# Kernel optimization log

Measured on AMD Instinct MI355X. Metric: run time of the kernel, lower is better.

## Reference

```python
import jax, jax.numpy as jnp
import numpy as np

B, S, D = 2, 2048, 768
H = 12
HD = D // H


def setup_inputs() -> dict:
    key = jax.random.key(0)
    ks = jax.random.split(key, 9)
    s_in = 1.0 / np.sqrt(D)
    return {
        "x": jax.random.normal(ks[0], (B, S, D), dtype=jnp.float32),
        "wq": jax.random.normal(ks[1], (D, D), dtype=jnp.float32) * s_in,
        "bq": jax.random.normal(ks[2], (D,), dtype=jnp.float32) * 0.01,
        "wk": jax.random.normal(ks[3], (D, D), dtype=jnp.float32) * s_in,
        "bk": jax.random.normal(ks[4], (D,), dtype=jnp.float32) * 0.01,
        "wv": jax.random.normal(ks[5], (D, D), dtype=jnp.float32) * s_in,
        "bv": jax.random.normal(ks[6], (D,), dtype=jnp.float32) * 0.01,
        "wo": jax.random.normal(ks[7], (D, D), dtype=jnp.float32) * s_in,
        "bo": jax.random.normal(ks[8], (D,), dtype=jnp.float32) * 0.01,
    }


def reference(x, wq, bq, wk, bk, wv, bv, wo, bo):
    b, s, _ = x.shape
    # projections -> [b, h, s, hd]
    def proj(w, bias):
        return (x @ w + bias).reshape(b, s, H, HD).transpose(0, 2, 1, 3)
    q = proj(wq, bq)
    k = proj(wk, bk)
    v = proj(wv, bv)
    scores = jnp.einsum("bhqd,bhkd->bhqk", q, k)
    causal = jnp.triu(jnp.ones((s, s), dtype=bool), k=1)
    scores = jnp.where(causal, -jnp.inf, scores)
    attn = jax.nn.softmax(scores / np.sqrt(HD), axis=-1)
    # dropout p=0.0 -> identity
    ctx = jnp.einsum("bhqk,bhkd->bhqd", attn, v)
    ctx = ctx.transpose(0, 2, 1, 3).reshape(b, s, D)
    return ctx @ wo + bo
```

## Files before the change

### kernel.cpp

```cpp
#include <hip/hip_runtime.h>
#include <math.h>

#define BB  2
#define SS  2048
#define DD  768
#define HH  12
#define HDD 64
#define BSR (BB * SS)
#define NCH 40
#define NKT 12

typedef __attribute__((ext_vector_type(8))) short bf16x8;
typedef __attribute__((ext_vector_type(4))) float f32x4;
typedef __attribute__((ext_vector_type(4))) int  i32x4;

__device__ inline f32x4 mfma16(bf16x8 a, bf16x8 b, f32x4 c) {
    return __builtin_amdgcn_mfma_f32_16x16x32_bf16(a, b, c, 0, 0, 0);
}

__device__ inline unsigned short f2b(float f) {
    unsigned int u = __float_as_uint(f);
    u += 0x7FFFu + ((u >> 16) & 1u);
    return (unsigned short)(u >> 16);
}
__device__ inline float b2f(unsigned short u) {
    return __uint_as_float((unsigned int)u << 16);
}

__device__ inline unsigned int cvt_pk_bf16(float lo, float hi) {
    unsigned int r;
    asm("v_cvt_pk_bf16_f32 %0, %1, %2" : "=v"(r) : "v"(lo), "v"(hi));
    return r;
}

__device__ inline void async_copy16(void* lds, const void* g) {
    __builtin_amdgcn_global_load_lds(
        (const __attribute__((address_space(1))) unsigned int*)g,
        (__attribute__((address_space(3))) unsigned int*)lds, 16, 0, 0);
}

__global__ __launch_bounds__(256) void conv_x_kernel(
    const float* __restrict__ x, unsigned short* __restrict__ xb)
{
    const size_t i = ((size_t)blockIdx.x * 256 + threadIdx.x) * 8;
    float4 f0 = *(const float4*)&x[i];
    float4 f1 = *(const float4*)&x[i + 4];
    i32x4 tv;
    tv[0] = (int)cvt_pk_bf16(f0.x, f0.y);
    tv[1] = (int)cvt_pk_bf16(f0.z, f0.w);
    tv[2] = (int)cvt_pk_bf16(f1.x, f1.y);
    tv[3] = (int)cvt_pk_bf16(f1.z, f1.w);
    *(i32x4*)&xb[i] = tv;
}

__global__ __launch_bounds__(256) void conv_wT_kernel(
    const float* __restrict__ w0, const float* __restrict__ w1,
    const float* __restrict__ w2, const float* __restrict__ w3,
    unsigned short* __restrict__ o0, unsigned short* __restrict__ o1,
    unsigned short* __restrict__ o2, unsigned short* __restrict__ o3)
{
    const float* w = (blockIdx.z == 0) ? w0 : (blockIdx.z == 1) ? w1
                   : (blockIdx.z == 2) ? w2 : w3;
    unsigned short* o = (blockIdx.z == 0) ? o0 : (blockIdx.z == 1) ? o1
                      : (blockIdx.z == 2) ? o2 : o3;
    const int n0 = blockIdx.x * 64;
    const int k0 = blockIdx.y * 64;
    const int tid = threadIdx.x;

    __shared__ unsigned short tile[64][72];

#pragma unroll
    for (int p = 0; p < 4; ++p) {
        int c  = p * 256 + tid;
        int kr = c >> 4;
        int nc = (c & 15) * 4;
        float4 v = *(const float4*)&w[(size_t)(k0 + kr) * DD + n0 + nc];
        tile[nc + 0][kr] = f2b(v.x);
        tile[nc + 1][kr] = f2b(v.y);
        tile[nc + 2][kr] = f2b(v.z);
        tile[nc + 3][kr] = f2b(v.w);
    }
    __syncthreads();
#pragma unroll
    for (int p = 0; p < 2; ++p) {
        int c  = p * 256 + tid;
        int nr = c >> 3;
        int kc = (c & 7) * 8;
        *(i32x4*)&o[(size_t)(n0 + nr) * DD + k0 + kc] = *(const i32x4*)&tile[nr][kc];
    }
}

__global__ __launch_bounds__(256) void qkv_gemm_kernel(
    const unsigned short* __restrict__ xb,
    const unsigned short* __restrict__ wqT, const unsigned short* __restrict__ wkT,
    const unsigned short* __restrict__ wvT,
    const float* __restrict__ bq, const float* __restrict__ bk,
    const float* __restrict__ bv,
    unsigned short* __restrict__ Qg, unsigned short* __restrict__ Kg,
    unsigned short* __restrict__ Vg)
{
    const int p0   = blockIdx.x;
    const int xcd  = p0 & 7;
    const int slot = p0 >> 3;
    const int m_t  = (slot / 18) * 8 + xcd;
    const int nw   = slot % 18;
    const int n_t  = nw / 3;
    const int which = nw % 3;

    const unsigned short* Bt = (which == 0) ? wqT : (which == 1) ? wkT : wvT;
    const float* bias        = (which == 0) ? bq  : (which == 1) ? bk  : bv;
    unsigned short* out      = (which == 0) ? Qg  : (which == 1) ? Kg  : Vg;
    const float qs           = (which == 0) ? 0.18033688011112042f : 1.0f;

    const int m0 = m_t * 64;
    const int n0 = n_t * 128;
    const int tid  = threadIdx.x;
    const int w    = tid >> 6;
    const int lane = tid & 63;
    const int quad = lane >> 4;
    const int l16  = lane & 15;
    const int mh   = w & 1;
    const int nh   = w >> 1;
    const int swz  = l16 & 7;

    __shared__ unsigned short smem[24576];
    unsigned short (*As0)[64] = (unsigned short(*)[64])smem;
    unsigned short (*Bs0)[64] = (unsigned short(*)[64])(smem + 4096);
    unsigned short (*As1)[64] = (unsigned short(*)[64])(smem + 12288);
    unsigned short (*Bs1)[64] = (unsigned short(*)[64])(smem + 16384);
    unsigned short (*T)[136]  = (unsigned short(*)[136])smem;

    const unsigned short* gA[2];
    int ldsA[2];
#pragma unroll
    for (int p = 0; p < 2; ++p) {
        int c  = p * 256 + tid;
        int r  = c >> 3;
        int j  = c & 7;
        int ch = j ^ (r & 7);
        gA[p]   = &xb[(size_t)(m0 + r) * DD + ch * 8];
        ldsA[p] = r * 64 + j * 8;
    }
    const unsigned short* gB[4];
    int ldsB[4];
#pragma unroll
    for (int p = 0; p < 4; ++p) {
        int c  = p * 256 + tid;
        int r  = c >> 3;
        int j  = c & 7;
        int ch = j ^ (r & 7);
        gB[p]   = &Bt[(size_t)(n0 + r) * DD + ch * 8];
        ldsB[p] = r * 64 + j * 8;
    }

    f32x4 zero = {0.f, 0.f, 0.f, 0.f};
    f32x4 acc[2][4];
#pragma unroll
    for (int i = 0; i < 2; ++i)
#pragma unroll
        for (int j = 0; j < 4; ++j) acc[i][j] = zero;

#pragma unroll
    for (int p = 0; p < 2; ++p) async_copy16((unsigned short*)As0 + ldsA[p], gA[p]);
#pragma unroll
    for (int p = 0; p < 4; ++p) async_copy16((unsigned short*)Bs0 + ldsB[p], gB[p]);
    __syncthreads();

#pragma unroll
    for (int t = 0; t < NKT; ++t) {
        const int kn = (t + 1) * 64;
        unsigned short (*As)[64] = (t & 1) ? As1 : As0;
        unsigned short (*Bs)[64] = (t & 1) ? Bs1 : Bs0;
        unsigned short (*An)[64] = (t & 1) ? As0 : As1;
        unsigned short (*Bn)[64] = (t & 1) ? Bs0 : Bs1;
        if (t + 1 < NKT) {
#pragma unroll
            for (int p = 0; p < 2; ++p)
                async_copy16((unsigned short*)An + ldsA[p], gA[p] + kn);
#pragma unroll
            for (int p = 0; p < 4; ++p)
                async_copy16((unsigned short*)Bn + ldsB[p], gB[p] + kn);
        }
        bf16x8 af0[2], af1[2], bf0[4], bf1[4];
#pragma unroll
        for (int mt = 0; mt < 2; ++mt) {
            int r = mh * 32 + mt * 16 + l16;
            af0[mt] = *(const bf16x8*)&As[r][((quad    ) ^ swz) * 8];
            af1[mt] = *(const bf16x8*)&As[r][((quad + 4) ^ swz) * 8];
        }
#pragma unroll
        for (int nt = 0; nt < 4; ++nt) {
            int r = nh * 64 + nt * 16 + l16;
            bf0[nt] = *(const bf16x8*)&Bs[r][((quad    ) ^ swz) * 8];
            bf1[nt] = *(const bf16x8*)&Bs[r][((quad + 4) ^ swz) * 8];
        }
#pragma unroll
        for (int mt = 0; mt < 2; ++mt)
#pragma unroll
            for (int nt = 0; nt < 4; ++nt) {
                acc[mt][nt] = mfma16(af0[mt], bf0[nt], acc[mt][nt]);
                acc[mt][nt] = mfma16(af1[mt], bf1[nt], acc[mt][nt]);
            }
        __syncthreads();
    }

    if (which < 2) {
#pragma unroll
        for (int nt = 0; nt < 4; ++nt) {
            const int col = nh * 64 + nt * 16 + l16;
            const float bvv = bias[n0 + col];
#pragma unroll
            for (int mt = 0; mt < 2; ++mt)
#pragma unroll
                for (int r = 0; r < 4; ++r)
                    T[mh * 32 + mt * 16 + quad * 4 + r][col] =
                        f2b((acc[mt][nt][r] + bvv) * qs);
        }
        __syncthreads();
#pragma unroll
        for (int p2 = 0; p2 < 4; ++p2) {
            int c    = p2 * 256 + tid;
            int row  = c >> 4;
            int ck   = c & 15;
            int head = ck >> 3;
            int wi   = ck & 7;
            int sg   = m0 + row;
            int bi   = sg >> 11, si = sg & 2047;
            int hcol = (n0 >> 6) + head;
            *(i32x4*)&out[(((size_t)(bi * HH + hcol)) * SS + si) * HDD + wi * 8] =
                *(const i32x4*)&T[row][head * 64 + wi * 8];
        }
    } else {
        for (int pass = 0; pass < 2; ++pass) {
            if (pass) __syncthreads();
            if (nh == pass) {
#pragma unroll
                for (int nt = 0; nt < 4; ++nt) {
                    const float bvv = bias[n0 + pass * 64 + nt * 16 + l16];
#pragma unroll
                    for (int mt = 0; mt < 2; ++mt) {
                        uint2 pk;
                        pk.x = cvt_pk_bf16(acc[mt][nt][0] + bvv, acc[mt][nt][1] + bvv);
                        pk.y = cvt_pk_bf16(acc[mt][nt][2] + bvv, acc[mt][nt][3] + bvv);
                        *(uint2*)&T[nt * 16 + l16][mh * 32 + mt * 16 + quad * 4] = pk;
                    }
                }
            }
            __syncthreads();
            const int bi   = m0 >> 11;
            const int s0   = m0 & 2047;
            const int hcol = (n0 >> 6) + pass;
#pragma unroll
            for (int p2 = 0; p2 < 2; ++p2) {
                int c    = p2 * 256 + tid;
                int drow = c >> 3;
                int wi   = c & 7;
                *(i32x4*)&out[(((size_t)(bi * HH + hcol)) * HDD + drow) * SS + s0 + wi * 8] =
                    *(const i32x4*)&T[drow][wi * 8];
            }
        }
    }
}

__global__ __launch_bounds__(256) void out_gemm_kernel(
    const unsigned short* __restrict__ cb, const unsigned short* __restrict__ woT,
    const float* __restrict__ bo, float* __restrict__ out)
{
    const int p0   = blockIdx.x;
    const int xcd  = p0 & 7;
    const int slot = p0 >> 3;
    const int m0 = ((slot / 6) * 8 + xcd) * 64;
    const int n0 = (slot % 6) * 128;
    const int tid  = threadIdx.x;
    const int w    = tid >> 6;
    const int lane = tid & 63;
    const int quad = lane >> 4;
    const int l16  = lane & 15;
    const int mh   = w & 1;
    const int nh   = w >> 1;
    const int swz  = l16 & 7;

    __shared__ unsigned short smem[24576];
    unsigned short (*As0)[64] = (unsigned short(*)[64])smem;
    unsigned short (*Bs0)[64] = (unsigned short(*)[64])(smem + 4096);
    unsigned short (*As1)[64] = (unsigned short(*)[64])(smem + 12288);
    unsigned short (*Bs1)[64] = (unsigned short(*)[64])(smem + 16384);

    const unsigned short* gA[2];
    int ldsA[2];
#pragma unroll
    for (int p = 0; p < 2; ++p) {
        int c  = p * 256 + tid;
        int r  = c >> 3;
        int j  = c & 7;
        int ch = j ^ (r & 7);
        gA[p]   = &cb[(size_t)(m0 + r) * DD + ch * 8];
        ldsA[p] = r * 64 + j * 8;
    }
    const unsigned short* gB[4];
    int ldsB[4];
#pragma unroll
    for (int p = 0; p < 4; ++p) {
        int c  = p * 256 + tid;
        int r  = c >> 3;
        int j  = c & 7;
        int ch = j ^ (r & 7);
        gB[p]   = &woT[(size_t)(n0 + r) * DD + ch * 8];
        ldsB[p] = r * 64 + j * 8;
    }

    f32x4 zero = {0.f, 0.f, 0.f, 0.f};
    f32x4 acc[2][4];
#pragma unroll
    for (int i = 0; i < 2; ++i)
#pragma unroll
        for (int j = 0; j < 4; ++j) acc[i][j] = zero;

#pragma unroll
    for (int p = 0; p < 2; ++p) async_copy16((unsigned short*)As0 + ldsA[p], gA[p]);
#pragma unroll
    for (int p = 0; p < 4; ++p) async_copy16((unsigned short*)Bs0 + ldsB[p], gB[p]);
    __syncthreads();

#pragma unroll
    for (int t = 0; t < NKT; ++t) {
        const int kn = (t + 1) * 64;
        unsigned short (*As)[64] = (t & 1) ? As1 : As0;
        unsigned short (*Bs)[64] = (t & 1) ? Bs1 : Bs0;
        unsigned short (*An)[64] = (t & 1) ? As0 : As1;
        unsigned short (*Bn)[64] = (t & 1) ? Bs0 : Bs1;
        if (t + 1 < NKT) {
#pragma unroll
            for (int p = 0; p < 2; ++p)
                async_copy16((unsigned short*)An + ldsA[p], gA[p] + kn);
#pragma unroll
            for (int p = 0; p < 4; ++p)
                async_copy16((unsigned short*)Bn + ldsB[p], gB[p] + kn);
        }
        bf16x8 af0[2], af1[2], bf0[4], bf1[4];
#pragma unroll
        for (int mt = 0; mt < 2; ++mt) {
            int r = mh * 32 + mt * 16 + l16;
            af0[mt] = *(const bf16x8*)&As[r][((quad    ) ^ swz) * 8];
            af1[mt] = *(const bf16x8*)&As[r][((quad + 4) ^ swz) * 8];
        }
#pragma unroll
        for (int nt = 0; nt < 4; ++nt) {
            int r = nh * 64 + nt * 16 + l16;
            bf0[nt] = *(const bf16x8*)&Bs[r][((quad    ) ^ swz) * 8];
            bf1[nt] = *(const bf16x8*)&Bs[r][((quad + 4) ^ swz) * 8];
        }
#pragma unroll
        for (int mt = 0; mt < 2; ++mt)
#pragma unroll
            for (int nt = 0; nt < 4; ++nt) {
                acc[mt][nt] = mfma16(af0[mt], bf0[nt], acc[mt][nt]);
                acc[mt][nt] = mfma16(af1[mt], bf1[nt], acc[mt][nt]);
            }
        __syncthreads();
    }

#pragma unroll
    for (int nt = 0; nt < 4; ++nt) {
        const int n = n0 + nh * 64 + nt * 16 + l16;
        const float bvv = bo[n];
#pragma unroll
        for (int mt = 0; mt < 2; ++mt) {
            const int mbase = m0 + mh * 32 + mt * 16 + quad * 4;
#pragma unroll
            for (int r = 0; r < 4; ++r)
                out[(size_t)(mbase + r) * DD + n] = acc[mt][nt][r] + bvv;
        }
    }
}

__global__ __launch_bounds__(256, 4) void attn_mfma_kernel(
    const unsigned short* __restrict__ Qg, const unsigned short* __restrict__ Kg,
    const unsigned short* __restrict__ Vg, unsigned short* __restrict__ Opart,
    float* __restrict__ Lb)
{
    const int p0   = blockIdx.x;
    const int xcd  = p0 & 7;
    const int slot = p0 >> 3;
    const int bh_i = (slot / 40) * 8 + xcd;
    const int b    = bh_i / HH;
    const int h    = bh_i % HH;
    const int c    = (NCH - 1) - (slot % 40);

    int qt, ck, nch;
    if (c < 4)       { qt = c;                            ck = 0;     nch = 1; }
    else if (c < 12) { int t = c - 4;  qt = 4  + (t >> 1); ck = t & 1; nch = 2; }
    else if (c < 24) { int t = c - 12; qt = 8  + t / 3;    ck = t % 3; nch = 3; }
    else             { int t = c - 24; qt = 12 + (t >> 2); ck = t & 3; nch = 4; }
    const int NT   = 2 * qt + 2;
    const int base = NT / nch, rem = NT % nch;
    const int lo   = ck * base + min(ck, rem);
    const int hi   = lo + base + (ck < rem ? 1 : 0);
    const int dlo  = 2 * qt;

    const int tid  = threadIdx.x;
    const int w    = tid >> 6;
    const int lane = tid & 63;
    const int quad = lane >> 4;
    const int l16  = lane & 15;
    const int q0   = qt * 128;

    const size_t bh = (size_t)bh_i;
    const unsigned short* qp = Qg + bh * SS * HDD;
    const unsigned short* kp = Kg + bh * SS * HDD;
    const unsigned short* vp = Vg + bh * HDD * SS;

    unsigned short* op = Opart + ((size_t)bh * NCH + c) * 128 * HDD;
    float* lp = Lb + ((size_t)bh * NCH + c) * 128;

    __shared__ unsigned short Ks[64][64];
    __shared__ unsigned short Vt[64][64];
    __shared__ unsigned short PsT[4][2][16][72];
    unsigned short* slab = &PsT[w][0][0][0];

    bf16x8 qb0[2], qb1[2];
    int query[2];
#pragma unroll
    for (int qf = 0; qf < 2; ++qf) {
        query[qf] = q0 + w * 32 + qf * 16 + l16;
        qb0[qf] = *(const bf16x8*)&qp[(size_t)query[qf] * HDD + quad * 8];
        qb1[qf] = *(const bf16x8*)&qp[(size_t)query[qf] * HDD + 32 + quad * 8];
    }

    const int pr  = tid >> 3;
    const int po8 = tid & 7;
    const int fs  = l16 & 7;

    i32x4 kpre[2], vpre[2];
#pragma unroll
    for (int p = 0; p < 2; ++p) {
        int r  = pr + p * 32;
        int gc = (po8 ^ (r & 7)) * 8;
        kpre[p] = *(const i32x4*)&kp[(size_t)(lo * 64 + r) * HDD + gc];
        vpre[p] = *(const i32x4*)&vp[(size_t)r * SS + lo * 64 + gc];
    }

    f32x4 zero = {0.f, 0.f, 0.f, 0.f};
    f32x4 o_acc[2][4];
    float l_i[2] = {0.f, 0.f};
#pragma unroll
    for (int qf = 0; qf < 2; ++qf)
#pragma unroll
        for (int i = 0; i < 4; ++i) o_acc[qf][i] = zero;

    for (int kt = lo; kt < hi; ++kt) {
        const int k0 = kt * 64;
        __syncthreads();
#pragma unroll
        for (int p = 0; p < 2; ++p) {
            int r = pr + p * 32;
            *(i32x4*)&Ks[r][po8 * 8] = kpre[p];
            *(i32x4*)&Vt[r][po8 * 8] = vpre[p];
        }
        __syncthreads();

        if (kt + 1 < hi) {
            const int kn = (kt + 1) * 64;
#pragma unroll
            for (int p = 0; p < 2; ++p) {
                int r  = pr + p * 32;
                int gc = (po8 ^ (r & 7)) * 8;
                kpre[p] = *(const i32x4*)&kp[(size_t)(kn + r) * HDD + gc];
                vpre[p] = *(const i32x4*)&vp[(size_t)r * SS + kn + gc];
            }
        }

        const bool diag = (kt >= dlo);
#pragma unroll
        for (int t = 0; t < 4; ++t) {
            const int row = t * 16 + l16;
            bf16x8 klo = *(const bf16x8*)&Ks[row][((quad    ) ^ fs) * 8];
            bf16x8 khi = *(const bf16x8*)&Ks[row][((quad + 4) ^ fs) * 8];
#pragma unroll
            for (int qf = 0; qf < 2; ++qf) {
                f32x4 s = mfma16(klo, qb0[qf], zero);
                s = mfma16(khi, qb1[qf], s);
                float pv[4];
#pragma unroll
                for (int r = 0; r < 4; ++r) {
                    const int key = k0 + t * 16 + quad * 4 + r;
                    float p = exp2f(s[r]);
                    if (diag && key > query[qf]) p = 0.f;
                    pv[r] = p;
                    l_i[qf] += p;
                }
                uint2 pk;
                pk.x = cvt_pk_bf16(pv[0], pv[1]);
                pk.y = cvt_pk_bf16(pv[2], pv[3]);
                *(uint2*)&slab[(qf * 16 + l16) * 72 + t * 16 + quad * 4] = pk;
            }
        }

        bf16x8 pb0[2], pb1[2];
#pragma unroll
        for (int qf = 0; qf < 2; ++qf) {
            pb0[qf] = *(const bf16x8*)&slab[(qf * 16 + l16) * 72 + quad * 8];
            pb1[qf] = *(const bf16x8*)&slab[(qf * 16 + l16) * 72 + 32 + quad * 8];
        }
#pragma unroll
        for (int t2 = 0; t2 < 4; ++t2) {
            const int row = t2 * 16 + l16;
            bf16x8 vlo = *(const bf16x8*)&Vt[row][((quad    ) ^ fs) * 8];
            bf16x8 vhi = *(const bf16x8*)&Vt[row][((quad + 4) ^ fs) * 8];
#pragma unroll
            for (int qf = 0; qf < 2; ++qf) {
                o_acc[qf][t2] = mfma16(vlo, pb0[qf], o_acc[qf][t2]);
                o_acc[qf][t2] = mfma16(vhi, pb1[qf], o_acc[qf][t2]);
            }
        }
    }

#pragma unroll
    for (int qf = 0; qf < 2; ++qf) {
        float l = l_i[qf];
        l += __shfl_xor(l, 16);
        l += __shfl_xor(l, 32);
        if (quad == 0) lp[w * 32 + qf * 16 + l16] = l;
#pragma unroll
        for (int t2 = 0; t2 < 4; ++t2) {
            uint2 pk;
            pk.x = cvt_pk_bf16(o_acc[qf][t2][0], o_acc[qf][t2][1]);
            pk.y = cvt_pk_bf16(o_acc[qf][t2][2], o_acc[qf][t2][3]);
            *(uint2*)&slab[(qf * 16 + l16) * 72 + t2 * 16 + quad * 4] = pk;
        }
    }
#pragma unroll
    for (int p2 = 0; p2 < 4; ++p2) {
        int cc  = p2 * 64 + lane;
        int row = cc >> 3, dc = cc & 7;
        *(i32x4*)&op[(size_t)(w * 32 + row) * HDD + dc * 8] =
            *(const i32x4*)&slab[row * 72 + dc * 8];
    }
}

__global__ __launch_bounds__(256) void merge_kernel(
    const unsigned short* __restrict__ Opart, const float* __restrict__ Lb,
    unsigned short* __restrict__ cb)
{
    const int bx   = blockIdx.x;
    const int qt2  = bx >> 1;
    const int half = bx & 1;
    const int bhn  = blockIdx.y;
    const int b    = bhn / HH, h = bhn % HH;
    const int tid  = threadIdx.x;
    const int row  = tid >> 2;
    const int d0   = (tid & 3) * 16;
    const int rowc = half * 64 + row;
    const int q    = qt2 * 128 + rowc;

    const int nch = (qt2 < 4) ? 1 : (qt2 < 8) ? 2 : (qt2 < 12) ? 3 : 4;
    const int cb0 = (qt2 < 4) ? qt2
                  : (qt2 < 8)  ? (4  + (qt2 - 4)  * 2)
                  : (qt2 < 12) ? (12 + (qt2 - 8)  * 3)
                  :              (24 + (qt2 - 12) * 4);

    float suml = 0.f;
    float accv[16];
#pragma unroll
    for (int i = 0; i < 16; ++i) accv[i] = 0.f;

    for (int ci = 0; ci < nch; ++ci) {
        const size_t base = (size_t)bhn * NCH + cb0 + ci;
        suml += Lb[base * 128 + rowc];
        const unsigned short* o = Opart + (base * 128 + rowc) * HDD + d0;
        i32x4 va = *(const i32x4*)&o[0];
        i32x4 vb = *(const i32x4*)&o[8];
#pragma unroll
        for (int wd = 0; wd < 4; ++wd) {
            unsigned int ua = (unsigned int)va[wd];
            accv[wd * 2 + 0] += __uint_as_float(ua << 16);
            accv[wd * 2 + 1] += __uint_as_float(ua & 0xffff0000u);
            unsigned int ub = (unsigned int)vb[wd];
            accv[8 + wd * 2 + 0] += __uint_as_float(ub << 16);
            accv[8 + wd * 2 + 1] += __uint_as_float(ub & 0xffff0000u);
        }
    }
    const float inv = 1.0f / suml;
    unsigned int res[8];
#pragma unroll
    for (int i = 0; i < 8; ++i)
        res[i] = cvt_pk_bf16(accv[2 * i] * inv, accv[2 * i + 1] * inv);
    unsigned short* dst = &cb[((size_t)(b * SS + q)) * DD + h * HDD + d0];
    *(i32x4*)&dst[0] = *(const i32x4*)&res[0];
    *(i32x4*)&dst[8] = *(const i32x4*)&res[4];
}

extern "C" void kernel_launch(void* const* d_in, const int* in_sizes, int n_in,
                              void* d_out, int out_size, void* d_ws, size_t ws_size,
                              hipStream_t stream)
{
    const float* x  = (const float*)d_in[0];
    const float* wq = (const float*)d_in[1];
    const float* bq = (const float*)d_in[2];
    const float* wk = (const float*)d_in[3];
    const float* bk = (const float*)d_in[4];
    const float* wv = (const float*)d_in[5];
    const float* bv = (const float*)d_in[6];
    const float* wo = (const float*)d_in[7];
    const float* bo = (const float*)d_in[8];
    float* out = (float*)d_out;

    char* p = (char*)d_ws;
    const size_t XB  = (size_t)BSR * DD * 2;
    const size_t WB  = (size_t)DD * DD * 2;
    const size_t OPB = (size_t)BB * HH * NCH * 128 * HDD * 2;
    const size_t LBB = (size_t)BB * HH * NCH * 128 * 4;
    unsigned short* wqT = (unsigned short*)p;            p += WB;
    unsigned short* wkT = (unsigned short*)p;            p += WB;
    unsigned short* wvT = (unsigned short*)p;            p += WB;
    unsigned short* woT = (unsigned short*)p;            p += WB;
    unsigned short* xb  = (unsigned short*)p;            p += XB;
    unsigned short* Qg  = (unsigned short*)p;            p += XB;
    unsigned short* Kg  = (unsigned short*)p;            p += XB;
    unsigned short* Vg  = (unsigned short*)p;            p += XB;
    unsigned short* cb  = (unsigned short*)p;            p += XB;
    unsigned short* Opart = (unsigned short*)p;          p += OPB;
    float* Lb = (float*)p;                               p += LBB;

    conv_x_kernel<<<dim3(BSR * DD / (256 * 8)), 256, 0, stream>>>(x, xb);
    conv_wT_kernel<<<dim3(DD / 64, DD / 64, 4), 256, 0, stream>>>(
        wq, wk, wv, wo, wqT, wkT, wvT, woT);
    qkv_gemm_kernel<<<dim3(1152), 256, 0, stream>>>(
        xb, wqT, wkT, wvT, bq, bk, bv, Qg, Kg, Vg);
    attn_mfma_kernel<<<dim3(960), 256, 0, stream>>>(
        Qg, Kg, Vg, Opart, Lb);
    merge_kernel<<<dim3(32, BB * HH), 256, 0, stream>>>(Opart, Lb, cb);
    out_gemm_kernel<<<dim3(384), 256, 0, stream>>>(cb, woT, bo, out);
}
```

Measured before the change: 153.2 us.

## Double-buffer K/V shared tiles in attention and split diagonal mask path

Turns the single K/V shared-memory tile into a two-slot ping-pong buffer. The next tile is written to shared memory and the tile after that is prefetched into registers while the current tile is being computed, which cuts the two block barriers per key tile down to one. The causal mask check now runs only on diagonal tiles, and launch bounds drop from 4 to 3 blocks per SM. The larger LDS footprint and lower occupancy target may reduce how many blocks stay resident at once.

```diff
diff --git a/kernel.cpp b/kernel.cpp
--- a/kernel.cpp
+++ b/kernel.cpp
@@ -374,7 +374,7 @@
     }
 }
 
-__global__ __launch_bounds__(256, 4) void attn_mfma_kernel(
+__global__ __launch_bounds__(256, 3) void attn_mfma_kernel(
     const unsigned short* __restrict__ Qg, const unsigned short* __restrict__ Kg,
     const unsigned short* __restrict__ Vg, unsigned short* __restrict__ Opart,
     float* __restrict__ Lb)
@@ -383,8 +383,6 @@
     const int xcd  = p0 & 7;
     const int slot = p0 >> 3;
     const int bh_i = (slot / 40) * 8 + xcd;
-    const int b    = bh_i / HH;
-    const int h    = bh_i % HH;
     const int c    = (NCH - 1) - (slot % 40);
 
     int qt, ck, nch;
@@ -413,8 +411,8 @@
     unsigned short* op = Opart + ((size_t)bh * NCH + c) * 128 * HDD;
     float* lp = Lb + ((size_t)bh * NCH + c) * 128;
 
-    __shared__ unsigned short Ks[64][64];
-    __shared__ unsigned short Vt[64][64];
+    __shared__ unsigned short Ks[2][64][64];
+    __shared__ unsigned short Vt[2][64][64];
     __shared__ unsigned short PsT[4][2][16][72];
     unsigned short* slab = &PsT[w][0][0][0];
 
@@ -439,6 +437,23 @@
         kpre[p] = *(const i32x4*)&kp[(size_t)(lo * 64 + r) * HDD + gc];
         vpre[p] = *(const i32x4*)&vp[(size_t)r * SS + lo * 64 + gc];
     }
+#pragma unroll
+    for (int p = 0; p < 2; ++p) {
+        int r = pr + p * 32;
+        *(i32x4*)&Ks[0][r][po8 * 8] = kpre[p];
+        *(i32x4*)&Vt[0][r][po8 * 8] = vpre[p];
+    }
+    if (lo + 1 < hi) {
+        const int kn = (lo + 1) * 64;
+#pragma unroll
+        for (int p = 0; p < 2; ++p) {
+            int r  = pr + p * 32;
+            int gc = (po8 ^ (r & 7)) * 8;
+            kpre[p] = *(const i32x4*)&kp[(size_t)(kn + r) * HDD + gc];
+            vpre[p] = *(const i32x4*)&vp[(size_t)r * SS + kn + gc];
+        }
+    }
+    __syncthreads();
 
     f32x4 zero = {0.f, 0.f, 0.f, 0.f};
     f32x4 o_acc[2][4];
@@ -449,24 +464,26 @@
         for (int i = 0; i < 4; ++i) o_acc[qf][i] = zero;
 
     for (int kt = lo; kt < hi; ++kt) {
-        const int k0 = kt * 64;
-        __syncthreads();
-#pragma unroll
-        for (int p = 0; p < 2; ++p) {
-            int r = pr + p * 32;
-            *(i32x4*)&Ks[r][po8 * 8] = kpre[p];
-            *(i32x4*)&Vt[r][po8 * 8] = vpre[p];
-        }
-        __syncthreads();
+        const int k0   = kt * 64;
+        const int bufc = (kt - lo) & 1;
+        const int bufn = bufc ^ 1;
 
         if (kt + 1 < hi) {
-            const int kn = (kt + 1) * 64;
 #pragma unroll
             for (int p = 0; p < 2; ++p) {
-                int r  = pr + p * 32;
-                int gc = (po8 ^ (r & 7)) * 8;
-                kpre[p] = *(const i32x4*)&kp[(size_t)(kn + r) * HDD + gc];
-                vpre[p] = *(const i32x4*)&vp[(size_t)r * SS + kn + gc];
+                int r = pr + p * 32;
+                *(i32x4*)&Ks[bufn][r][po8 * 8] = kpre[p];
+                *(i32x4*)&Vt[bufn][r][po8 * 8] = vpre[p];
+            }
+            if (kt + 2 < hi) {
+                const int kn = (kt + 2) * 64;
+#pragma unroll
+                for (int p = 0; p < 2; ++p) {
+                    int r  = pr + p * 32;
+                    int gc = (po8 ^ (r & 7)) * 8;
+                    kpre[p] = *(const i32x4*)&kp[(size_t)(kn + r) * HDD + gc];
+                    vpre[p] = *(const i32x4*)&vp[(size_t)r * SS + kn + gc];
+                }
             }
         }
 
@@ -474,20 +491,28 @@
 #pragma unroll
         for (int t = 0; t < 4; ++t) {
             const int row = t * 16 + l16;
-            bf16x8 klo = *(const bf16x8*)&Ks[row][((quad    ) ^ fs) * 8];
-            bf16x8 khi = *(const bf16x8*)&Ks[row][((quad + 4) ^ fs) * 8];
+            bf16x8 klo = *(const bf16x8*)&Ks[bufc][row][((quad    ) ^ fs) * 8];
+            bf16x8 khi = *(const bf16x8*)&Ks[bufc][row][((quad + 4) ^ fs) * 8];
 #pragma unroll
             for (int qf = 0; qf < 2; ++qf) {
                 f32x4 s = mfma16(klo, qb0[qf], zero);
                 s = mfma16(khi, qb1[qf], s);
                 float pv[4];
-#pragma unroll
-                for (int r = 0; r < 4; ++r) {
-                    const int key = k0 + t * 16 + quad * 4 + r;
-                    float p = exp2f(s[r]);
-                    if (diag && key > query[qf]) p = 0.f;
-                    pv[r] = p;
-                    l_i[qf] += p;
+                if (!diag) {
+#pragma unroll
+                    for (int r = 0; r < 4; ++r) {
+                        pv[r] = exp2f(s[r]);
+                        l_i[qf] += pv[r];
+                    }
+                } else {
+#pragma unroll
+                    for (int r = 0; r < 4; ++r) {
+                        const int key = k0 + t * 16 + quad * 4 + r;
+                        float p = exp2f(s[r]);
+                        if (key > query[qf]) p = 0.f;
+                        pv[r] = p;
+                        l_i[qf] += p;
+                    }
                 }
                 uint2 pk;
                 pk.x = cvt_pk_bf16(pv[0], pv[1]);
@@ -505,14 +530,16 @@
 #pragma unroll
         for (int t2 = 0; t2 < 4; ++t2) {
             const int row = t2 * 16 + l16;
-            bf16x8 vlo = *(const bf16x8*)&Vt[row][((quad    ) ^ fs) * 8];
-            bf16x8 vhi = *(const bf16x8*)&Vt[row][((quad + 4) ^ fs) * 8];
+            bf16x8 vlo = *(const bf16x8*)&Vt[bufc][row][((quad    ) ^ fs) * 8];
+            bf16x8 vhi = *(const bf16x8*)&Vt[bufc][row][((quad + 4) ^ fs) * 8];
 #pragma unroll
             for (int qf = 0; qf < 2; ++qf) {
                 o_acc[qf][t2] = mfma16(vlo, pb0[qf], o_acc[qf][t2]);
                 o_acc[qf][t2] = mfma16(vhi, pb1[qf], o_acc[qf][t2]);
             }
         }
+
+        if (kt + 1 < hi) __syncthreads();
     }
 
 #pragma unroll
```

Measured after the change: 156.4 us. 1.02x slower.

## Fuse split-KV merge into output projection GEMM A-tile loading

Applied to the files above, without the earlier changes.

Removes the separate merge kernel and the cb context buffer. The output GEMM now reads partial attention outputs and row sums directly, combines and normalises them in registers, and writes the bf16 A tile into shared memory, prefetching the next head's partials during the current MFMA step. This saves one launch and a global round trip for the context tensor. In exchange, the GEMM's A loads become synchronous register loads with extra ALU work, replacing async copies, and each row's merge is redone by all six N-column blocks.

```diff
diff --git a/kernel.cpp b/kernel.cpp
--- a/kernel.cpp
+++ b/kernel.cpp
@@ -263,7 +263,8 @@
 }
 
 __global__ __launch_bounds__(256) void out_gemm_kernel(
-    const unsigned short* __restrict__ cb, const unsigned short* __restrict__ woT,
+    const unsigned short* __restrict__ Opart, const float* __restrict__ Lb,
+    const unsigned short* __restrict__ woT,
     const float* __restrict__ bo, float* __restrict__ out)
 {
     const int p0   = blockIdx.x;
@@ -280,23 +281,33 @@
     const int nh   = w >> 1;
     const int swz  = l16 & 7;
 
+    const int bi   = m0 >> 11;
+    const int s0   = m0 & 2047;
+    const int qt2  = s0 >> 7;
+    const int half = (s0 >> 6) & 1;
+    const int nch = (qt2 < 4) ? 1 : (qt2 < 8) ? 2 : (qt2 < 12) ? 3 : 4;
+    const int cb0 = (qt2 < 4) ? qt2
+                  : (qt2 < 8)  ? (4  + (qt2 - 4)  * 2)
+                  : (qt2 < 12) ? (12 + (qt2 - 8)  * 3)
+                  :              (24 + (qt2 - 12) * 4);
+
     __shared__ unsigned short smem[24576];
     unsigned short (*As0)[64] = (unsigned short(*)[64])smem;
     unsigned short (*Bs0)[64] = (unsigned short(*)[64])(smem + 4096);
     unsigned short (*As1)[64] = (unsigned short(*)[64])(smem + 12288);
     unsigned short (*Bs1)[64] = (unsigned short(*)[64])(smem + 16384);
 
-    const unsigned short* gA[2];
-    int ldsA[2];
-#pragma unroll
-    for (int p = 0; p < 2; ++p) {
-        int c  = p * 256 + tid;
-        int r  = c >> 3;
-        int j  = c & 7;
-        int ch = j ^ (r & 7);
-        gA[p]   = &cb[(size_t)(m0 + r) * DD + ch * 8];
-        ldsA[p] = r * 64 + j * 8;
-    }
+    const int arow = tid >> 2;
+    const int ad0  = (tid & 3) * 16;
+    const int aj0  = ad0 >> 3;
+    const int aw0  = arow * 64 + ((aj0      ^ (arow & 7)) * 8);
+    const int aw1  = arow * 64 + (((aj0 + 1) ^ (arow & 7)) * 8);
+    const size_t rstep = (size_t)NCH * 128;
+    size_t rbase[4];
+#pragma unroll
+    for (int ci = 0; ci < 4; ++ci)
+        rbase[ci] = ((size_t)(bi * HH) * NCH + cb0 + ci) * 128 + half * 64 + arow;
+
     const unsigned short* gB[4];
     int ldsB[4];
 #pragma unroll
@@ -316,10 +327,43 @@
 #pragma unroll
         for (int j = 0; j < 4; ++j) acc[i][j] = zero;
 
-#pragma unroll
-    for (int p = 0; p < 2; ++p) async_copy16((unsigned short*)As0 + ldsA[p], gA[p]);
+    i32x4 pa[4][2];
+    float pl[4];
+
+#pragma unroll
+    for (int ci = 0; ci < 4; ++ci) if (ci < nch) {
+        const unsigned short* o = Opart + rbase[ci] * HDD + ad0;
+        pa[ci][0] = *(const i32x4*)&o[0];
+        pa[ci][1] = *(const i32x4*)&o[8];
+        pl[ci] = Lb[rbase[ci]];
+    }
 #pragma unroll
     for (int p = 0; p < 4; ++p) async_copy16((unsigned short*)Bs0 + ldsB[p], gB[p]);
+    {
+        float suml = 0.f, a16[16];
+#pragma unroll
+        for (int i = 0; i < 16; ++i) a16[i] = 0.f;
+#pragma unroll
+        for (int ci = 0; ci < 4; ++ci) if (ci < nch) {
+            suml += pl[ci];
+#pragma unroll
+            for (int wd = 0; wd < 4; ++wd) {
+                unsigned int ua = (unsigned int)pa[ci][0][wd];
+                a16[wd * 2 + 0] += __uint_as_float(ua << 16);
+                a16[wd * 2 + 1] += __uint_as_float(ua & 0xffff0000u);
+                unsigned int ub = (unsigned int)pa[ci][1][wd];
+                a16[8 + wd * 2 + 0] += __uint_as_float(ub << 16);
+                a16[8 + wd * 2 + 1] += __uint_as_float(ub & 0xffff0000u);
+            }
+        }
+        const float inv = 1.0f / suml;
+        unsigned int res[8];
+#pragma unroll
+        for (int i = 0; i < 8; ++i)
+            res[i] = cvt_pk_bf16(a16[2 * i] * inv, a16[2 * i + 1] * inv);
+        *(i32x4*)((unsigned short*)As0 + aw0) = *(const i32x4*)&res[0];
+        *(i32x4*)((unsigned short*)As0 + aw1) = *(const i32x4*)&res[4];
+    }
     __syncthreads();
 
 #pragma unroll
@@ -329,14 +373,22 @@
         unsigned short (*Bs)[64] = (t & 1) ? Bs1 : Bs0;
         unsigned short (*An)[64] = (t & 1) ? As0 : As1;
         unsigned short (*Bn)[64] = (t & 1) ? Bs0 : Bs1;
-        if (t + 1 < NKT) {
-#pragma unroll
-            for (int p = 0; p < 2; ++p)
-                async_copy16((unsigned short*)An + ldsA[p], gA[p] + kn);
+        const bool more = (t + 1 < NKT);
+
+        if (more) {
+#pragma unroll
+            for (int ci = 0; ci < 4; ++ci) if (ci < nch) {
+                const size_t rr = rbase[ci] + (size_t)(t + 1) * rstep;
+                const unsigned short* o = Opart + rr * HDD + ad0;
+                pa[ci][0] = *(const i32x4*)&o[0];
+                pa[ci][1] = *(const i32x4*)&o[8];
+                pl[ci] = Lb[rr];
+            }
 #pragma unroll
             for (int p = 0; p < 4; ++p)
                 async_copy16((unsigned short*)Bn + ldsB[p], gB[p] + kn);
         }
+
         bf16x8 af0[2], af1[2], bf0[4], bf1[4];
 #pragma unroll
         for (int mt = 0; mt < 2; ++mt) {
@@ -357,6 +409,32 @@
                 acc[mt][nt] = mfma16(af0[mt], bf0[nt], acc[mt][nt]);
                 acc[mt][nt] = mfma16(af1[mt], bf1[nt], acc[mt][nt]);
             }
+
+        if (more) {
+            float suml = 0.f, a16[16];
+#pragma unroll
+            for (int i = 0; i < 16; ++i) a16[i] = 0.f;
+#pragma unroll
+            for (int ci = 0; ci < 4; ++ci) if (ci < nch) {
+                suml += pl[ci];
+#pragma unroll
+                for (int wd = 0; wd < 4; ++wd) {
+                    unsigned int ua = (unsigned int)pa[ci][0][wd];
+                    a16[wd * 2 + 0] += __uint_as_float(ua << 16);
+                    a16[wd * 2 + 1] += __uint_as_float(ua & 0xffff0000u);
+                    unsigned int ub = (unsigned int)pa[ci][1][wd];
+                    a16[8 + wd * 2 + 0] += __uint_as_float(ub << 16);
+                    a16[8 + wd * 2 + 1] += __uint_as_float(ub & 0xffff0000u);
+                }
+            }
+            const float inv = 1.0f / suml;
+            unsigned int res[8];
+#pragma unroll
+            for (int i = 0; i < 8; ++i)
+                res[i] = cvt_pk_bf16(a16[2 * i] * inv, a16[2 * i + 1] * inv);
+            *(i32x4*)((unsigned short*)An + aw0) = *(const i32x4*)&res[0];
+            *(i32x4*)((unsigned short*)An + aw1) = *(const i32x4*)&res[4];
+        }
         __syncthreads();
     }
 
@@ -383,8 +461,6 @@
     const int xcd  = p0 & 7;
     const int slot = p0 >> 3;
     const int bh_i = (slot / 40) * 8 + xcd;
-    const int b    = bh_i / HH;
-    const int h    = bh_i % HH;
     const int c    = (NCH - 1) - (slot % 40);
 
     int qt, ck, nch;
@@ -536,58 +612,6 @@
         *(i32x4*)&op[(size_t)(w * 32 + row) * HDD + dc * 8] =
             *(const i32x4*)&slab[row * 72 + dc * 8];
     }
-}
-
-__global__ __launch_bounds__(256) void merge_kernel(
-    const unsigned short* __restrict__ Opart, const float* __restrict__ Lb,
-    unsigned short* __restrict__ cb)
-{
-    const int bx   = blockIdx.x;
-    const int qt2  = bx >> 1;
-    const int half = bx & 1;
-    const int bhn  = blockIdx.y;
-    const int b    = bhn / HH, h = bhn % HH;
-    const int tid  = threadIdx.x;
-    const int row  = tid >> 2;
-    const int d0   = (tid & 3) * 16;
-    const int rowc = half * 64 + row;
-    const int q    = qt2 * 128 + rowc;
-
-    const int nch = (qt2 < 4) ? 1 : (qt2 < 8) ? 2 : (qt2 < 12) ? 3 : 4;
-    const int cb0 = (qt2 < 4) ? qt2
-                  : (qt2 < 8)  ? (4  + (qt2 - 4)  * 2)
-                  : (qt2 < 12) ? (12 + (qt2 - 8)  * 3)
-                  :              (24 + (qt2 - 12) * 4);
-
-    float suml = 0.f;
-    float accv[16];
-#pragma unroll
-    for (int i = 0; i < 16; ++i) accv[i] = 0.f;
-
-    for (int ci = 0; ci < nch; ++ci) {
-        const size_t base = (size_t)bhn * NCH + cb0 + ci;
-        suml += Lb[base * 128 + rowc];
-        const unsigned short* o = Opart + (base * 128 + rowc) * HDD + d0;
-        i32x4 va = *(const i32x4*)&o[0];
-        i32x4 vb = *(const i32x4*)&o[8];
-#pragma unroll
-        for (int wd = 0; wd < 4; ++wd) {
-            unsigned int ua = (unsigned int)va[wd];
-            accv[wd * 2 + 0] += __uint_as_float(ua << 16);
-            accv[wd * 2 + 1] += __uint_as_float(ua & 0xffff0000u);
-            unsigned int ub = (unsigned int)vb[wd];
-            accv[8 + wd * 2 + 0] += __uint_as_float(ub << 16);
-            accv[8 + wd * 2 + 1] += __uint_as_float(ub & 0xffff0000u);
-        }
-    }
-    const float inv = 1.0f / suml;
-    unsigned int res[8];
-#pragma unroll
-    for (int i = 0; i < 8; ++i)
-        res[i] = cvt_pk_bf16(accv[2 * i] * inv, accv[2 * i + 1] * inv);
-    unsigned short* dst = &cb[((size_t)(b * SS + q)) * DD + h * HDD + d0];
-    *(i32x4*)&dst[0] = *(const i32x4*)&res[0];
-    *(i32x4*)&dst[8] = *(const i32x4*)&res[4];
 }
 
 extern "C" void kernel_launch(void* const* d_in, const int* in_sizes, int n_in,
@@ -618,7 +642,6 @@
     unsigned short* Qg  = (unsigned short*)p;            p += XB;
     unsigned short* Kg  = (unsigned short*)p;            p += XB;
     unsigned short* Vg  = (unsigned short*)p;            p += XB;
-    unsigned short* cb  = (unsigned short*)p;            p += XB;
     unsigned short* Opart = (unsigned short*)p;          p += OPB;
     float* Lb = (float*)p;                               p += LBB;
 
@@ -629,6 +652,5 @@
         xb, wqT, wkT, wvT, bq, bk, bv, Qg, Kg, Vg);
     attn_mfma_kernel<<<dim3(960), 256, 0, stream>>>(
         Qg, Kg, Vg, Opart, Lb);
-    merge_kernel<<<dim3(32, BB * HH), 256, 0, stream>>>(Opart, Lb, cb);
-    out_gemm_kernel<<<dim3(384), 256, 0, stream>>>(cb, woT, bo, out);
-}
+    out_gemm_kernel<<<dim3(384), 256, 0, stream>>>(Opart, Lb, woT, bo, out);
+}
```

Result: slower. 158.8 us (+3.7%).
